# Performance work log

Measured on AMD Instinct MI355X. Metric: run time of the kernel, lower is better.

## Reference

```python
import jax, jax.numpy as jnp
import numpy as np

E = 256   # embed_dim
H = 8     # num_heads
D = E // H  # head_dim = 32
L = 1024  # seq len (Q_len == K_len == V_len)


def setup_inputs() -> dict:
    key = jax.random.key(0)
    ks = jax.random.split(key, 10)
    f = lambda k, s: jax.random.normal(k, s, dtype=jnp.float32)
    return {
        "V": f(ks[0], (L, E)),
        "K": f(ks[1], (L, E)),
        "Q": f(ks[2], (L, E)),
        # genomic-style coordinates, strictly positive
        "position": jax.random.uniform(ks[3], (L,), dtype=jnp.float32) * 1e5,
        "Wq": f(ks[4], (E, E)) * 0.02,
        "Wk": f(ks[5], (E, E)) * 0.02,
        "Wv": f(ks[6], (E, E)) * 0.02,
        "Wr": f(ks[7], (E, 1)) * 0.02,   # K_relative_linear weight [out=E, in=1]
        "Wo": f(ks[8], (E, E)) * 0.02,
        "bo": jnp.zeros((E,), jnp.float32),
    }


def reference(V, K, Q, position, Wq, Wk, Wv, Wr, Wo, bo):
    Lq = Q.shape[0]
    # projections (nn.Linear: x @ W.T), split into heads -> (L, H, D)
    q = (Q @ Wq.T).reshape(Lq, H, D)
    k = (K @ Wk.T).reshape(Lq, H, D)
    v = (V @ Wv.T).reshape(Lq, H, D)

    # relative position scalar per (q, k) pair: log(|p_q - p_k| + 1)
    rel = jnp.log(jnp.abs(position[:, None] - position[None, :]) + 1.0)  # (L, L)

    # K_relative_linear maps scalar rel -> (H, D); the einsum
    # 'nqhd,nhqjd->nhqj' then factorizes exactly as:
    #   sum_d Q[q,h,d] * rel[q,j] * Wr[h,d] = (Q . Wr)[h,q] * rel[q,j]
    # so we avoid materializing the (H, L, L, D) tensor while computing
    # mathematically identical results.
    Wr_h = Wr[:, 0].reshape(H, D)                    # (H, D)
    coeff = jnp.einsum('qhd,hd->hq', q, Wr_h)        # (H, L)

    energy = jnp.einsum('qhd,khd->hqk', q, k)        # (H, L, L)
    energy = energy + coeff[:, :, None] * rel[None, :, :]

    attn = jax.nn.softmax(energy / np.float32(E) ** 0.5, axis=2)
    out = jnp.einsum('hqk,khd->qhd', attn, v).reshape(Lq, E)
    out = out @ Wo.T + bo
    return out
```

## Files before the change

### kernel.cpp

```cpp
#include <hip/hip_runtime.h>
#include <math.h>

#define EDIM 256
#define LDIM 1024
#define HDIM 8
#define DDIM 32

typedef __attribute__((ext_vector_type(8))) short short8;
typedef __attribute__((ext_vector_type(4))) float f32x4;

__device__ inline unsigned short bf16h(float x) {
    unsigned u = __float_as_uint(x);
    return (unsigned short)((u + 0x7fff + ((u >> 16) & 1)) >> 16);
}
__device__ inline float bf16tof(unsigned short h) {
    return __uint_as_float(((unsigned)h) << 16);
}

__global__ __launch_bounds__(256) void proj_kernel(
    const float* __restrict__ Q, const float* __restrict__ Km, const float* __restrict__ V,
    const float* __restrict__ Wq, const float* __restrict__ Wk, const float* __restrict__ Wv,
    const float* __restrict__ Wr,
    float* __restrict__ qT, float* __restrict__ kT, float* __restrict__ vT,
    float* __restrict__ coeff)
{
    const int z = blockIdx.z;
    const float* __restrict__ X = (z == 0) ? Q : (z == 1) ? Km : V;
    const float* __restrict__ W = (z == 0) ? Wq : (z == 1) ? Wk : Wv;
    float* __restrict__ dst     = (z == 0) ? qT : (z == 1) ? kT : vT;

    const int n0 = blockIdx.x * 32;
    const int o0 = blockIdx.y * 32;
    const int tid = threadIdx.x;
    const int tx = tid & 15, ty = tid >> 4;

    __shared__ float Xs[32][34];
    __shared__ float Ws[32][34];

    float acc[2][2] = {{0.f,0.f},{0.f,0.f}};

    const int sn  = tid >> 3;
    const int sc4 = (tid & 7) * 4;

    float4 xa = *(const float4*)(X + (n0 + sn) * EDIM + sc4);
    float4 wa = *(const float4*)(W + (o0 + sn) * EDIM + sc4);

    for (int kb = 0; kb < EDIM; kb += 32) {
        __syncthreads();
        Xs[sc4+0][sn]=xa.x; Xs[sc4+1][sn]=xa.y; Xs[sc4+2][sn]=xa.z; Xs[sc4+3][sn]=xa.w;
        Ws[sc4+0][sn]=wa.x; Ws[sc4+1][sn]=wa.y; Ws[sc4+2][sn]=wa.z; Ws[sc4+3][sn]=wa.w;
        float4 xn, wn;
        if (kb + 32 < EDIM) {
            xn = *(const float4*)(X + (n0 + sn) * EDIM + kb + 32 + sc4);
            wn = *(const float4*)(W + (o0 + sn) * EDIM + kb + 32 + sc4);
        }
        __syncthreads();
        #pragma unroll
        for (int e = 0; e < 32; ++e) {
            float2 x2 = *(const float2*)&Xs[e][ty*2];
            float2 w2 = *(const float2*)&Ws[e][tx*2];
            acc[0][0] += x2.x*w2.x; acc[0][1] += x2.x*w2.y;
            acc[1][0] += x2.y*w2.x; acc[1][1] += x2.y*w2.y;
        }
        xa = xn; wa = wn;
    }

    const int h = o0 >> 5;
    #pragma unroll
    for (int i = 0; i < 2; ++i) {
        const int n = n0 + ty*2 + i;
        float2 r; r.x = acc[i][0]; r.y = acc[i][1];
        *(float2*)(dst + h*(LDIM*DDIM) + n*DDIM + tx*2) = r;
    }

    if (z == 0) {
        const float wr0 = Wr[o0 + tx*2], wr1 = Wr[o0 + tx*2 + 1];
        #pragma unroll
        for (int i = 0; i < 2; ++i) {
            float c = acc[i][0]*wr0 + acc[i][1]*wr1;
            c += __shfl_xor(c, 1, 64);
            c += __shfl_xor(c, 2, 64);
            c += __shfl_xor(c, 4, 64);
            c += __shfl_xor(c, 8, 64);
            if (tx == 0) coeff[h*LDIM + n0 + ty*2 + i] = c;
        }
    }
}

__global__ __launch_bounds__(256, 4) void attn_kernel(
    const float* __restrict__ qT, const float* __restrict__ kT, const float* __restrict__ vT,
    const float* __restrict__ coeff, const float* __restrict__ pos,
    float* __restrict__ Op, float* __restrict__ Mp, float* __restrict__ Lp, int nkt)
{
    const int h   = blockIdx.y;
    const int q0  = blockIdx.x * 64;
    const int p   = blockIdx.z;
    const int kt0 = p * nkt * 64;
    const int tid  = threadIdx.x;
    const int wave = tid >> 6;
    const int lane = tid & 63;
    const int n    = lane & 15;
    const int quad = lane >> 4;
    const int qs0  = wave * 16;

    __shared__ __align__(16) short khi[4*64*8];
    __shared__ __align__(16) short klo[4*64*8];
    __shared__ float vs[64][36];
    __shared__ float ps_t[64][68];
    __shared__ float alph[64];
    __shared__ float pk[64];

    short8 qhi, qlo;
    {
        const float* qp = qT + (h*LDIM + q0 + qs0 + n) * DDIM + quad*8;
        float4 qa = *(const float4*)qp;
        float4 qb = *(const float4*)(qp + 4);
        float v[8] = {qa.x,qa.y,qa.z,qa.w, qb.x,qb.y,qb.z,qb.w};
        #pragma unroll
        for (int j = 0; j < 8; ++j) {
            unsigned short hh = bf16h(v[j]);
            qhi[j] = (short)hh;
            qlo[j] = (short)bf16h(v[j] - bf16tof(hh));
        }
    }

    float pq[4], cq[4];
    #pragma unroll
    for (int i = 0; i < 4; ++i) {
        const int r = q0 + qs0 + 4*quad + i;
        pq[i] = pos[r];
        cq[i] = coeff[h*LDIM + r] * 0.0625f;
    }

    float m[4], l[4];
    #pragma unroll
    for (int i = 0; i < 4; ++i) { m[i] = -INFINITY; l[i] = 0.f; }

    const int pr0 = (tid >> 4) * 4;
    const int dg2 = (tid & 15) * 2;
    float o[4][2];
    #pragma unroll
    for (int i = 0; i < 4; ++i) { o[i][0] = 0.f; o[i][1] = 0.f; }

    const int cS = tid >> 2;
    const int dq = tid & 3;
    const int lane2 = (cS & 15) | (dq << 4);
    const int gS = cS >> 4;

    float4 k0c, k1c, v0c, v1c; float pkc = 0.f;
    {
        const float* kp = kT + (h*LDIM + kt0 + cS) * DDIM + dq*8;
        k0c = *(const float4*)kp; k1c = *(const float4*)(kp + 4);
        const float* vp = vT + (h*LDIM + kt0 + cS) * DDIM + dq*8;
        v0c = *(const float4*)vp; v1c = *(const float4*)(vp + 4);
        if (tid < 64) pkc = pos[kt0 + tid];
    }

    for (int t = 0; t < nkt; ++t) {
        __syncthreads();

        {
            float kv[8] = {k0c.x,k0c.y,k0c.z,k0c.w, k1c.x,k1c.y,k1c.z,k1c.w};
            short8 hi8, lo8;
            #pragma unroll
            for (int j = 0; j < 8; ++j) {
                unsigned short hh = bf16h(kv[j]);
                hi8[j] = (short)hh;
                lo8[j] = (short)bf16h(kv[j] - bf16tof(hh));
            }
            *((short8*)&khi[(gS*64 + lane2)*8]) = hi8;
            *((short8*)&klo[(gS*64 + lane2)*8]) = lo8;
            *(float4*)&vs[cS][dq*8]     = v0c;
            *(float4*)&vs[cS][dq*8 + 4] = v1c;
            if (tid < 64) pk[tid] = pkc;
        }

        float4 k0n, k1n, v0n, v1n; float pkn = 0.f;
        if (t + 1 < nkt) {
            const int kt = kt0 + (t+1) * 64;
            const float* kp = kT + (h*LDIM + kt + cS) * DDIM + dq*8;
            k0n = *(const float4*)kp; k1n = *(const float4*)(kp + 4);
            const float* vp = vT + (h*LDIM + kt + cS) * DDIM + dq*8;
            v0n = *(const float4*)vp; v1n = *(const float4*)(vp + 4);
            if (tid < 64) pkn = pos[kt + tid];
        }
        __syncthreads();

        f32x4 Sf[4];
        #pragma unroll
        for (int t4 = 0; t4 < 4; ++t4) {
            short8 bhi = *((const short8*)&khi[(t4*64 + lane)*8]);
            short8 blo = *((const short8*)&klo[(t4*64 + lane)*8]);
            f32x4 acc = {0.f, 0.f, 0.f, 0.f};
            acc = __builtin_amdgcn_mfma_f32_16x16x32_bf16(qlo, bhi, acc, 0, 0, 0);
            acc = __builtin_amdgcn_mfma_f32_16x16x32_bf16(qhi, blo, acc, 0, 0, 0);
            acc = __builtin_amdgcn_mfma_f32_16x16x32_bf16(qhi, bhi, acc, 0, 0, 0);
            Sf[t4] = acc;
        }

        float ev[4][4];
        float rmax[4] = {-INFINITY, -INFINITY, -INFINITY, -INFINITY};
        #pragma unroll
        for (int t4 = 0; t4 < 4; ++t4) {
            const float pkt = pk[16*t4 + n];
            #pragma unroll
            for (int i = 0; i < 4; ++i) {
                float s = fmaf(Sf[t4][i], 0.0625f, cq[i] * __logf(fabsf(pq[i] - pkt) + 1.f));
                ev[t4][i] = s;
                rmax[i] = fmaxf(rmax[i], s);
            }
        }
        #pragma unroll
        for (int off = 1; off < 16; off <<= 1)
            #pragma unroll
            for (int i = 0; i < 4; ++i)
                rmax[i] = fmaxf(rmax[i], __shfl_xor(rmax[i], off, 64));

        float al[4], rsum[4];
        #pragma unroll
        for (int i = 0; i < 4; ++i) {
            const float mn = fmaxf(m[i], rmax[i]);
            al[i] = __expf(m[i] - mn);
            m[i] = mn;
            rsum[i] = 0.f;
        }
        #pragma unroll
        for (int t4 = 0; t4 < 4; ++t4)
            #pragma unroll
            for (int i = 0; i < 4; ++i) {
                float e = __expf(ev[t4][i] - m[i]);
                ev[t4][i] = e;
                rsum[i] += e;
            }
        #pragma unroll
        for (int off = 1; off < 16; off <<= 1)
            #pragma unroll
            for (int i = 0; i < 4; ++i)
                rsum[i] += __shfl_xor(rsum[i], off, 64);
        #pragma unroll
        for (int i = 0; i < 4; ++i) l[i] = l[i]*al[i] + rsum[i];

        if (n == 0) {
            #pragma unroll
            for (int i = 0; i < 4; ++i) alph[qs0 + 4*quad + i] = al[i];
        }
        #pragma unroll
        for (int t4 = 0; t4 < 4; ++t4) {
            float4 w; w.x = ev[t4][0]; w.y = ev[t4][1]; w.z = ev[t4][2]; w.w = ev[t4][3];
            *(float4*)&ps_t[16*t4 + n][qs0 + 4*quad] = w;
        }
        __syncthreads();

        {
            float4 a4 = *(const float4*)&alph[pr0];
            o[0][0]*=a4.x; o[0][1]*=a4.x; o[1][0]*=a4.y; o[1][1]*=a4.y;
            o[2][0]*=a4.z; o[2][1]*=a4.z; o[3][0]*=a4.w; o[3][1]*=a4.w;
        }
        #pragma unroll 4
        for (int c = 0; c < 64; ++c) {
            float4 p4 = *(const float4*)&ps_t[c][pr0];
            float2 v2 = *(const float2*)&vs[c][dg2];
            o[0][0] += p4.x*v2.x; o[0][1] += p4.x*v2.y;
            o[1][0] += p4.y*v2.x; o[1][1] += p4.y*v2.y;
            o[2][0] += p4.z*v2.x; o[2][1] += p4.z*v2.y;
            o[3][0] += p4.w*v2.x; o[3][1] += p4.w*v2.y;
        }

        k0c = k0n; k1c = k1n; v0c = v0n; v1c = v1n; pkc = pkn;
    }

    const int ph = p * HDIM + h;
    #pragma unroll
    for (int i = 0; i < 4; ++i) {
        float2 w; w.x = o[i][0]; w.y = o[i][1];
        *(float2*)(Op + ((size_t)ph*LDIM + q0 + pr0 + i)*DDIM + dg2) = w;
    }
    if (n == 0) {
        #pragma unroll
        for (int i = 0; i < 4; ++i) {
            const int r = q0 + qs0 + 4*quad + i;
            Mp[ph*LDIM + r] = m[i];
            Lp[ph*LDIM + r] = l[i];
        }
    }
}

__global__ __launch_bounds__(256) void combine_kernel(
    const float* __restrict__ Op, const float* __restrict__ Mp, const float* __restrict__ Lp,
    int P, float* __restrict__ A)
{
    const int idx = blockIdx.x * 256 + threadIdx.x;
    const int n  = idx >> 6;
    const int e4 = (idx & 63) * 4;
    const int h  = e4 >> 5;
    const int d  = e4 & 31;

    float mv[8], lv[8];
    float mx = -INFINITY;
    #pragma unroll
    for (int p = 0; p < 8; ++p) if (p < P) {
        mv[p] = Mp[(p*HDIM + h)*LDIM + n];
        lv[p] = Lp[(p*HDIM + h)*LDIM + n];
        mx = fmaxf(mx, mv[p]);
    }
    float s = 0.f;
    #pragma unroll
    for (int p = 0; p < 8; ++p) if (p < P) {
        float a = __expf(mv[p] - mx);
        mv[p] = a;
        s += a * lv[p];
    }
    const float inv = 1.f / s;

    float4 x; x.x = x.y = x.z = x.w = 0.f;
    #pragma unroll
    for (int p = 0; p < 8; ++p) if (p < P) {
        const float sp = mv[p] * inv;
        float4 xp = *(const float4*)(Op + ((size_t)(p*HDIM + h)*LDIM + n)*DDIM + d);
        x.x += sp*xp.x; x.y += sp*xp.y; x.z += sp*xp.z; x.w += sp*xp.w;
    }
    *(float4*)(A + n*EDIM + e4) = x;
}

__global__ __launch_bounds__(256) void outproj_kernel(
    const float* __restrict__ A, const float* __restrict__ Wo,
    const float* __restrict__ bo, float* __restrict__ out)
{
    const int n0 = blockIdx.x * 32;
    const int o0 = blockIdx.y * 32;
    const int tid = threadIdx.x;
    const int tx = tid & 15, ty = tid >> 4;

    __shared__ float Xs[32][34];
    __shared__ float Ws[32][34];

    float acc[2][2] = {{0.f,0.f},{0.f,0.f}};

    const int sn  = tid >> 3;
    const int sc4 = (tid & 7) * 4;

    float4 xa = *(const float4*)(A  + (n0 + sn) * EDIM + sc4);
    float4 wa = *(const float4*)(Wo + (o0 + sn) * EDIM + sc4);

    for (int kb = 0; kb < EDIM; kb += 32) {
        __syncthreads();
        Xs[sc4+0][sn]=xa.x; Xs[sc4+1][sn]=xa.y; Xs[sc4+2][sn]=xa.z; Xs[sc4+3][sn]=xa.w;
        Ws[sc4+0][sn]=wa.x; Ws[sc4+1][sn]=wa.y; Ws[sc4+2][sn]=wa.z; Ws[sc4+3][sn]=wa.w;
        float4 xn, wn;
        if (kb + 32 < EDIM) {
            xn = *(const float4*)(A  + (n0 + sn) * EDIM + kb + 32 + sc4);
            wn = *(const float4*)(Wo + (o0 + sn) * EDIM + kb + 32 + sc4);
        }
        __syncthreads();
        #pragma unroll
        for (int e = 0; e < 32; ++e) {
            float2 x2 = *(const float2*)&Xs[e][ty*2];
            float2 w2 = *(const float2*)&Ws[e][tx*2];
            acc[0][0] += x2.x*w2.x; acc[0][1] += x2.x*w2.y;
            acc[1][0] += x2.y*w2.x; acc[1][1] += x2.y*w2.y;
        }
        xa = xn; wa = wn;
    }

    const int oo = o0 + tx*2;
    float2 bias = *(const float2*)(bo + oo);
    #pragma unroll
    for (int i = 0; i < 2; ++i) {
        const int nn = n0 + ty*2 + i;
        float2 r; r.x = acc[i][0] + bias.x; r.y = acc[i][1] + bias.y;
        *(float2*)(out + nn*EDIM + oo) = r;
    }
}

extern "C" void kernel_launch(void* const* d_in, const int* in_sizes, int n_in,
                              void* d_out, int out_size, void* d_ws, size_t ws_size,
                              hipStream_t stream) {
    const float* V   = (const float*)d_in[0];
    const float* K   = (const float*)d_in[1];
    const float* Q   = (const float*)d_in[2];
    const float* pos = (const float*)d_in[3];
    const float* Wq  = (const float*)d_in[4];
    const float* Wk  = (const float*)d_in[5];
    const float* Wv  = (const float*)d_in[6];
    const float* Wr  = (const float*)d_in[7];
    const float* Wo  = (const float*)d_in[8];
    const float* bo  = (const float*)d_in[9];
    float* out = (float*)d_out;
    float* ws  = (float*)d_ws;

    auto need = [](int P) -> size_t {
        return (size_t)(794624 + P*278528) * 4;
    };
    int P = 2;
    if (ws_size >= need(8)) P = 8;
    else if (ws_size >= need(4)) P = 4;

    float* qT    = ws;
    float* kT    = ws + 262144;
    float* vT    = ws + 524288;
    float* coeff = ws + 786432;
    float* Op    = ws + 794624;
    float* Mp    = Op + (size_t)P * 262144;
    float* Lp    = Mp + (size_t)P * 8192;
    float* A     = qT;

    proj_kernel   <<<dim3(32, 8, 3), 256, 0, stream>>>(Q, K, V, Wq, Wk, Wv, Wr, qT, kT, vT, coeff);
    attn_kernel   <<<dim3(16, 8, P), 256, 0, stream>>>(qT, kT, vT, coeff, pos, Op, Mp, Lp, 16 / P);
    combine_kernel<<<dim3(256),      256, 0, stream>>>(Op, Mp, Lp, P, A);
    outproj_kernel<<<dim3(32, 8),    256, 0, stream>>>(A, Wo, bo, out);
}
```

Baseline: 122.7 us.

## Use split-bf16 MFMA for input and output projections

Adds a conversion kernel that splits Q/K/V and the weight matrices into hi/lo bf16 pairs. The projection and output-projection kernels are rewritten to use 16x16x32 bf16 MFMA with three products per tile (hi*hi, hi*lo, lo*hi) instead of scalar FP32 FMA through shared memory. The combine kernel now emits the attention output as hi/lo bf16. This moves the GEMM work onto matrix cores at near-fp32 accuracy, but adds an extra kernel launch, extra memory traffic for the split copies, and a larger workspace requirement that could lower the chosen split count P.

```diff
diff --git a/kernel.cpp b/kernel.cpp
--- a/kernel.cpp
+++ b/kernel.cpp
@@ -7,6 +7,7 @@
 #define DDIM 32
 
 typedef __attribute__((ext_vector_type(8))) short short8;
+typedef __attribute__((ext_vector_type(4))) short short4v;
 typedef __attribute__((ext_vector_type(4))) float f32x4;
 
 __device__ inline unsigned short bf16h(float x) {
@@ -17,72 +18,118 @@
     return __uint_as_float(((unsigned)h) << 16);
 }
 
+__global__ __launch_bounds__(256) void convert_kernel(
+    const float* __restrict__ Q, const float* __restrict__ K, const float* __restrict__ V,
+    const float* __restrict__ Wq, const float* __restrict__ Wk, const float* __restrict__ Wv,
+    const float* __restrict__ Wo,
+    short* __restrict__ Qh, short* __restrict__ Ql, short* __restrict__ Kh, short* __restrict__ Kl,
+    short* __restrict__ Vh, short* __restrict__ Vl, short* __restrict__ Wqh, short* __restrict__ Wql,
+    short* __restrict__ Wkh, short* __restrict__ Wkl, short* __restrict__ Wvh, short* __restrict__ Wvl,
+    short* __restrict__ Woh, short* __restrict__ Wol)
+{
+    const int z = blockIdx.y;
+    const float* src; short* dh; short* dl; int cnt;
+    switch (z) {
+        case 0: src = Q;  dh = Qh;  dl = Ql;  cnt = LDIM*EDIM; break;
+        case 1: src = K;  dh = Kh;  dl = Kl;  cnt = LDIM*EDIM; break;
+        case 2: src = V;  dh = Vh;  dl = Vl;  cnt = LDIM*EDIM; break;
+        case 3: src = Wq; dh = Wqh; dl = Wql; cnt = EDIM*EDIM; break;
+        case 4: src = Wk; dh = Wkh; dl = Wkl; cnt = EDIM*EDIM; break;
+        case 5: src = Wv; dh = Wvh; dl = Wvl; cnt = EDIM*EDIM; break;
+        default: src = Wo; dh = Woh; dl = Wol; cnt = EDIM*EDIM; break;
+    }
+    const int idx = (blockIdx.x * 256 + threadIdx.x) * 8;
+    if (idx >= cnt) return;
+    float4 a = *(const float4*)(src + idx);
+    float4 b = *(const float4*)(src + idx + 4);
+    float v[8] = {a.x,a.y,a.z,a.w, b.x,b.y,b.z,b.w};
+    short8 hi, lo;
+    #pragma unroll
+    for (int j = 0; j < 8; ++j) {
+        unsigned short hh = bf16h(v[j]);
+        hi[j] = (short)hh;
+        lo[j] = (short)bf16h(v[j] - bf16tof(hh));
+    }
+    *(short8*)&dh[idx] = hi;
+    *(short8*)&dl[idx] = lo;
+}
+
 __global__ __launch_bounds__(256) void proj_kernel(
-    const float* __restrict__ Q, const float* __restrict__ Km, const float* __restrict__ V,
-    const float* __restrict__ Wq, const float* __restrict__ Wk, const float* __restrict__ Wv,
+    const short* __restrict__ Qh, const short* __restrict__ Ql,
+    const short* __restrict__ Kh, const short* __restrict__ Kl,
+    const short* __restrict__ Vh, const short* __restrict__ Vl,
+    const short* __restrict__ Wqh, const short* __restrict__ Wql,
+    const short* __restrict__ Wkh, const short* __restrict__ Wkl,
+    const short* __restrict__ Wvh, const short* __restrict__ Wvl,
     const float* __restrict__ Wr,
     float* __restrict__ qT, float* __restrict__ kT, float* __restrict__ vT,
     float* __restrict__ coeff)
 {
     const int z = blockIdx.z;
-    const float* __restrict__ X = (z == 0) ? Q : (z == 1) ? Km : V;
-    const float* __restrict__ W = (z == 0) ? Wq : (z == 1) ? Wk : Wv;
-    float* __restrict__ dst     = (z == 0) ? qT : (z == 1) ? kT : vT;
-
-    const int n0 = blockIdx.x * 32;
-    const int o0 = blockIdx.y * 32;
-    const int tid = threadIdx.x;
-    const int tx = tid & 15, ty = tid >> 4;
-
-    __shared__ float Xs[32][34];
-    __shared__ float Ws[32][34];
-
-    float acc[2][2] = {{0.f,0.f},{0.f,0.f}};
-
-    const int sn  = tid >> 3;
-    const int sc4 = (tid & 7) * 4;
-
-    float4 xa = *(const float4*)(X + (n0 + sn) * EDIM + sc4);
-    float4 wa = *(const float4*)(W + (o0 + sn) * EDIM + sc4);
-
+    const short* __restrict__ Xh = (z == 0) ? Qh : (z == 1) ? Kh : Vh;
+    const short* __restrict__ Xl = (z == 0) ? Ql : (z == 1) ? Kl : Vl;
+    const short* __restrict__ Wh = (z == 0) ? Wqh : (z == 1) ? Wkh : Wvh;
+    const short* __restrict__ Wl = (z == 0) ? Wql : (z == 1) ? Wkl : Wvl;
+    float* __restrict__ dst      = (z == 0) ? qT : (z == 1) ? kT : vT;
+
+    const int n0 = blockIdx.x * 64;
+    const int o0 = blockIdx.y * 64;
+    const int wave = threadIdx.x >> 6;
+    const int lane = threadIdx.x & 63;
+    const int n16  = lane & 15;
+    const int quad = lane >> 4;
+
+    const int mrow = n0 + wave*16 + n16;
+
+    f32x4 acc[4];
+    #pragma unroll
+    for (int t4 = 0; t4 < 4; ++t4) acc[t4] = (f32x4){0.f,0.f,0.f,0.f};
+
+    #pragma unroll 2
     for (int kb = 0; kb < EDIM; kb += 32) {
-        __syncthreads();
-        Xs[sc4+0][sn]=xa.x; Xs[sc4+1][sn]=xa.y; Xs[sc4+2][sn]=xa.z; Xs[sc4+3][sn]=xa.w;
-        Ws[sc4+0][sn]=wa.x; Ws[sc4+1][sn]=wa.y; Ws[sc4+2][sn]=wa.z; Ws[sc4+3][sn]=wa.w;
-        float4 xn, wn;
-        if (kb + 32 < EDIM) {
-            xn = *(const float4*)(X + (n0 + sn) * EDIM + kb + 32 + sc4);
-            wn = *(const float4*)(W + (o0 + sn) * EDIM + kb + 32 + sc4);
-        }
-        __syncthreads();
-        #pragma unroll
-        for (int e = 0; e < 32; ++e) {
-            float2 x2 = *(const float2*)&Xs[e][ty*2];
-            float2 w2 = *(const float2*)&Ws[e][tx*2];
-            acc[0][0] += x2.x*w2.x; acc[0][1] += x2.x*w2.y;
-            acc[1][0] += x2.y*w2.x; acc[1][1] += x2.y*w2.y;
-        }
-        xa = xn; wa = wn;
-    }
-
-    const int h = o0 >> 5;
-    #pragma unroll
-    for (int i = 0; i < 2; ++i) {
-        const int n = n0 + ty*2 + i;
-        float2 r; r.x = acc[i][0]; r.y = acc[i][1];
-        *(float2*)(dst + h*(LDIM*DDIM) + n*DDIM + tx*2) = r;
+        short8 ah = *(const short8*)&Xh[mrow*EDIM + kb + quad*8];
+        short8 al = *(const short8*)&Xl[mrow*EDIM + kb + quad*8];
+        #pragma unroll
+        for (int t4 = 0; t4 < 4; ++t4) {
+            const int orow = o0 + 16*t4 + n16;
+            short8 bh = *(const short8*)&Wh[orow*EDIM + kb + quad*8];
+            short8 bl = *(const short8*)&Wl[orow*EDIM + kb + quad*8];
+            acc[t4] = __builtin_amdgcn_mfma_f32_16x16x32_bf16(al, bh, acc[t4], 0, 0, 0);
+            acc[t4] = __builtin_amdgcn_mfma_f32_16x16x32_bf16(ah, bl, acc[t4], 0, 0, 0);
+            acc[t4] = __builtin_amdgcn_mfma_f32_16x16x32_bf16(ah, bh, acc[t4], 0, 0, 0);
+        }
+    }
+
+    #pragma unroll
+    for (int t4 = 0; t4 < 4; ++t4) {
+        const int o = o0 + 16*t4 + n16;
+        const int h = o >> 5, d = o & 31;
+        #pragma unroll
+        for (int i = 0; i < 4; ++i) {
+            const int r = n0 + wave*16 + quad*4 + i;
+            dst[h*(LDIM*DDIM) + r*DDIM + d] = acc[t4][i];
+        }
     }
 
     if (z == 0) {
-        const float wr0 = Wr[o0 + tx*2], wr1 = Wr[o0 + tx*2 + 1];
-        #pragma unroll
-        for (int i = 0; i < 2; ++i) {
-            float c = acc[i][0]*wr0 + acc[i][1]*wr1;
-            c += __shfl_xor(c, 1, 64);
-            c += __shfl_xor(c, 2, 64);
-            c += __shfl_xor(c, 4, 64);
-            c += __shfl_xor(c, 8, 64);
-            if (tx == 0) coeff[h*LDIM + n0 + ty*2 + i] = c;
+        float wr[4];
+        #pragma unroll
+        for (int t4 = 0; t4 < 4; ++t4) wr[t4] = Wr[o0 + 16*t4 + n16];
+        const int h0 = o0 >> 5;
+        #pragma unroll
+        for (int i = 0; i < 4; ++i) {
+            float c0 = acc[0][i]*wr[0] + acc[1][i]*wr[1];
+            float c1 = acc[2][i]*wr[2] + acc[3][i]*wr[3];
+            #pragma unroll
+            for (int off = 1; off < 16; off <<= 1) {
+                c0 += __shfl_xor(c0, off, 64);
+                c1 += __shfl_xor(c1, off, 64);
+            }
+            if (n16 == 0) {
+                const int r = n0 + wave*16 + quad*4 + i;
+                coeff[h0*LDIM + r]     = c0;
+                coeff[(h0+1)*LDIM + r] = c1;
+            }
         }
     }
 }
@@ -287,7 +334,7 @@
 
 __global__ __launch_bounds__(256) void combine_kernel(
     const float* __restrict__ Op, const float* __restrict__ Mp, const float* __restrict__ Lp,
-    int P, float* __restrict__ A)
+    int P, short* __restrict__ Ah, short* __restrict__ Al)
 {
     const int idx = blockIdx.x * 256 + threadIdx.x;
     const int n  = idx >> 6;
@@ -312,63 +359,66 @@
     }
     const float inv = 1.f / s;
 
-    float4 x; x.x = x.y = x.z = x.w = 0.f;
+    float x[4] = {0.f, 0.f, 0.f, 0.f};
     #pragma unroll
     for (int p = 0; p < 8; ++p) if (p < P) {
         const float sp = mv[p] * inv;
         float4 xp = *(const float4*)(Op + ((size_t)(p*HDIM + h)*LDIM + n)*DDIM + d);
-        x.x += sp*xp.x; x.y += sp*xp.y; x.z += sp*xp.z; x.w += sp*xp.w;
-    }
-    *(float4*)(A + n*EDIM + e4) = x;
+        x[0] += sp*xp.x; x[1] += sp*xp.y; x[2] += sp*xp.z; x[3] += sp*xp.w;
+    }
+    short4v hi, lo;
+    #pragma unroll
+    for (int j = 0; j < 4; ++j) {
+        unsigned short hh = bf16h(x[j]);
+        hi[j] = (short)hh;
+        lo[j] = (short)bf16h(x[j] - bf16tof(hh));
+    }
+    *(short4v*)&Ah[n*EDIM + e4] = hi;
+    *(short4v*)&Al[n*EDIM + e4] = lo;
 }
 
 __global__ __launch_bounds__(256) void outproj_kernel(
-    const float* __restrict__ A, const float* __restrict__ Wo,
+    const short* __restrict__ Ah, const short* __restrict__ Al,
+    const short* __restrict__ Woh, const short* __restrict__ Wol,
     const float* __restrict__ bo, float* __restrict__ out)
 {
-    const int n0 = blockIdx.x * 32;
-    const int o0 = blockIdx.y * 32;
-    const int tid = threadIdx.x;
-    const int tx = tid & 15, ty = tid >> 4;
-
-    __shared__ float Xs[32][34];
-    __shared__ float Ws[32][34];
-
-    float acc[2][2] = {{0.f,0.f},{0.f,0.f}};
-
-    const int sn  = tid >> 3;
-    const int sc4 = (tid & 7) * 4;
-
-    float4 xa = *(const float4*)(A  + (n0 + sn) * EDIM + sc4);
-    float4 wa = *(const float4*)(Wo + (o0 + sn) * EDIM + sc4);
-
+    const int n0 = blockIdx.x * 64;
+    const int o0 = blockIdx.y * 64;
+    const int wave = threadIdx.x >> 6;
+    const int lane = threadIdx.x & 63;
+    const int n16  = lane & 15;
+    const int quad = lane >> 4;
+
+    const int mrow = n0 + wave*16 + n16;
+
+    f32x4 acc[4];
+    #pragma unroll
+    for (int t4 = 0; t4 < 4; ++t4) acc[t4] = (f32x4){0.f,0.f,0.f,0.f};
+
+    #pragma unroll 2
     for (int kb = 0; kb < EDIM; kb += 32) {
-        __syncthreads();
-        Xs[sc4+0][sn]=xa.x; Xs[sc4+1][sn]=xa.y; Xs[sc4+2][sn]=xa.z; Xs[sc4+3][sn]=xa.w;
-        Ws[sc4+0][sn]=wa.x; Ws[sc4+1][sn]=wa.y; Ws[sc4+2][sn]=wa.z; Ws[sc4+3][sn]=wa.w;
-        float4 xn, wn;
-        if (kb + 32 < EDIM) {
-            xn = *(const float4*)(A  + (n0 + sn) * EDIM + kb + 32 + sc4);
-            wn = *(const float4*)(Wo + (o0 + sn) * EDIM + kb + 32 + sc4);
-        }
-        __syncthreads();
-        #pragma unroll
-        for (int e = 0; e < 32; ++e) {
-            float2 x2 = *(const float2*)&Xs[e][ty*2];
-            float2 w2 = *(const float2*)&Ws[e][tx*2];
-            acc[0][0] += x2.x*w2.x; acc[0][1] += x2.x*w2.y;
-            acc[1][0] += x2.y*w2.x; acc[1][1] += x2.y*w2.y;
-        }
-        xa = xn; wa = wn;
-    }
-
-    const int oo = o0 + tx*2;
-    float2 bias = *(const float2*)(bo + oo);
-    #pragma unroll
-    for (int i = 0; i < 2; ++i) {
-        const int nn = n0 + ty*2 + i;
-        float2 r; r.x = acc[i][0] + bias.x; r.y = acc[i][1] + bias.y;
-        *(float2*)(out + nn*EDIM + oo) = r;
+        short8 ah = *(const short8*)&Ah[mrow*EDIM + kb + quad*8];
+        short8 al = *(const short8*)&Al[mrow*EDIM + kb + quad*8];
+        #pragma unroll
+        for (int t4 = 0; t4 < 4; ++t4) {
+            const int orow = o0 + 16*t4 + n16;
+            short8 bh = *(const short8*)&Woh[orow*EDIM + kb + quad*8];
+            short8 bl = *(const short8*)&Wol[orow*EDIM + kb + quad*8];
+            acc[t4] = __builtin_amdgcn_mfma_f32_16x16x32_bf16(al, bh, acc[t4], 0, 0, 0);
+            acc[t4] = __builtin_amdgcn_mfma_f32_16x16x32_bf16(ah, bl, acc[t4], 0, 0, 0);
+            acc[t4] = __builtin_amdgcn_mfma_f32_16x16x32_bf16(ah, bh, acc[t4], 0, 0, 0);
+        }
+    }
+
+    #pragma unroll
+    for (int t4 = 0; t4 < 4; ++t4) {
+        const int o = o0 + 16*t4 + n16;
+        const float b = bo[o];
+        #pragma unroll
+        for (int i = 0; i < 4; ++i) {
+            const int r = n0 + wave*16 + quad*4 + i;
+            out[r*EDIM + o] = acc[t4][i] + b;
+        }
     }
 }
 
@@ -388,24 +438,37 @@
     float* out = (float*)d_out;
     float* ws  = (float*)d_ws;
 
+    float* base = ws;
+    short* Qh  = (short*)(base);            short* Ql  = (short*)(base + 131072);
+    short* Kh  = (short*)(base + 262144);   short* Kl  = (short*)(base + 393216);
+    short* Vh  = (short*)(base + 524288);   short* Vl  = (short*)(base + 655360);
+    short* Wqh = (short*)(base + 786432);   short* Wql = (short*)(base + 819200);
+    short* Wkh = (short*)(base + 851968);   short* Wkl = (short*)(base + 884736);
+    short* Wvh = (short*)(base + 917504);   short* Wvl = (short*)(base + 950272);
+    short* Woh = (short*)(base + 983040);   short* Wol = (short*)(base + 1015808);
+    float* qT    = base + 1048576;
+    float* kT    = base + 1310720;
+    float* vT    = base + 1572864;
+    float* coeff = base + 1835008;
+    short* Ah    = (short*)(base + 1843200);
+    short* Al    = (short*)(base + 1974272);
+    float* Op    = base + 2105344;
+
     auto need = [](int P) -> size_t {
-        return (size_t)(794624 + P*278528) * 4;
+        return (size_t)(2105344 + P*278528) * 4;
     };
     int P = 2;
     if (ws_size >= need(8)) P = 8;
     else if (ws_size >= need(4)) P = 4;
 
-    float* qT    = ws;
-    float* kT    = ws + 262144;
-    float* vT    = ws + 524288;
-    float* coeff = ws + 786432;
-    float* Op    = ws + 794624;
-    float* Mp    = Op + (size_t)P * 262144;
-    float* Lp    = Mp + (size_t)P * 8192;
-    float* A     = qT;
-
-    proj_kernel   <<<dim3(32, 8, 3), 256, 0, stream>>>(Q, K, V, Wq, Wk, Wv, Wr, qT, kT, vT, coeff);
+    float* Mp = Op + (size_t)P * 262144;
+    float* Lp = Mp + (size_t)P * 8192;
+
+    convert_kernel<<<dim3(128, 7),   256, 0, stream>>>(Q, K, V, Wq, Wk, Wv, Wo,
+        Qh, Ql, Kh, Kl, Vh, Vl, Wqh, Wql, Wkh, Wkl, Wvh, Wvl, Woh, Wol);
+    proj_kernel   <<<dim3(16, 4, 3), 256, 0, stream>>>(Qh, Ql, Kh, Kl, Vh, Vl,
+        Wqh, Wql, Wkh, Wkl, Wvh, Wvl, Wr, qT, kT, vT, coeff);
     attn_kernel   <<<dim3(16, 8, P), 256, 0, stream>>>(qT, kT, vT, coeff, pos, Op, Mp, Lp, 16 / P);
-    combine_kernel<<<dim3(256),      256, 0, stream>>>(Op, Mp, Lp, P, A);
-    outproj_kernel<<<dim3(32, 8),    256, 0, stream>>>(A, Wo, bo, out);
-}
+    combine_kernel<<<dim3(256),      256, 0, stream>>>(Op, Mp, Lp, P, Ah, Al);
+    outproj_kernel<<<dim3(16, 4),    256, 0, stream>>>(Ah, Al, Woh, Wol, bo, out);
+}
```

Measured after the change: 130.5 us. +6.3%, slower.
